# Optimization experiments

Hardware: AMD Instinct MI355X
Metric: run time of the kernel (lower is better)

The kernel has to match this reference:

```python
import jax, jax.numpy as jnp
import numpy as np

B, T, C = 4, 2048, 768
N_HEADS = 16
HEAD_DIM = C // N_HEADS  # 48
ROPE_BASE = 10000.0


def setup_inputs() -> dict:
    key = jax.random.key(0)
    ks = jax.random.split(key, 6)
    s = 0.02
    return {
        "hidden_states": jax.random.normal(ks[0], (B, T, C), dtype=jnp.float32),
        "attention_mask": jnp.ones((B, T), dtype=jnp.float32),
        "Wq": jax.random.normal(ks[1], (C, C), dtype=jnp.float32) * s,
        "bq": jnp.zeros((C,), dtype=jnp.float32),
        "Wk": jax.random.normal(ks[2], (C, C), dtype=jnp.float32) * s,
        "bk": jnp.zeros((C,), dtype=jnp.float32),
        "Wv": jax.random.normal(ks[3], (C, C), dtype=jnp.float32) * s,
        "bv": jnp.zeros((C,), dtype=jnp.float32),
        "Wo": jax.random.normal(ks[4], (C, C), dtype=jnp.float32) * s,
        "bo": jnp.zeros((C,), dtype=jnp.float32),
    }


def _rotate_half(x):
    x1, x2 = jnp.split(x, 2, axis=-1)
    return jnp.concatenate([-x2, x1], axis=-1)


def reference(hidden_states, attention_mask, Wq, bq, Wk, bk, Wv, bv, Wo, bo):
    b, t, c = hidden_states.shape
    h, d = N_HEADS, c // N_HEADS

    def split_heads(x):  # [b,t,c] -> [b,h,t,d]
        return x.reshape(b, t, h, d).transpose(0, 2, 1, 3)

    q = split_heads(hidden_states @ Wq.T + bq)
    k = split_heads(hidden_states @ Wk.T + bk)
    v = split_heads(hidden_states @ Wv.T + bv)

    # rotary embedding: cos/sin [t, d]
    pos = jnp.arange(t, dtype=jnp.float32)
    inv_freq = 1.0 / (ROPE_BASE ** (jnp.arange(0, d, 2, dtype=jnp.float32) / d))
    freqs = pos[:, None] * inv_freq[None, :]          # [t, d/2]
    emb = jnp.concatenate([freqs, freqs], axis=-1)    # [t, d]
    cos, sin = jnp.cos(emb), jnp.sin(emb)
    q = q * cos + _rotate_half(q) * sin
    k = k * cos + _rotate_half(k) * sin

    scores = jnp.einsum('bhqd,bhkd->bhqk', q, k) / jnp.sqrt(jnp.asarray(d, q.dtype))
    # additive padding mask: (1 - mask) * -10000, broadcast [b,1,1,t]
    scores = scores + (1.0 - attention_mask)[:, None, None, :] * -10000.0
    # causal mask with -inf
    causal = jnp.tril(jnp.ones((t, t), dtype=bool))
    scores = jnp.where(causal[None, None], scores, -jnp.inf)

    probs = jax.nn.softmax(scores, axis=-1)
    ctx = jnp.einsum('bhqk,bhkd->bhqd', probs, v)
    ctx = ctx.transpose(0, 2, 1, 3).reshape(b, t, c)
    return ctx @ Wo.T + bo
```

## Files before the change

### kernel.cpp

```cpp
#include <hip/hip_runtime.h>
#include <hip/hip_bf16.h>
#include <math.h>

#define BB 4
#define TT 2048
#define CC 768
#define NHD 16
#define HD 48
#define NQT 32

typedef __hip_bfloat16 bf16;
typedef __attribute__((ext_vector_type(8))) short short8;
typedef __attribute__((ext_vector_type(4))) float floatx4;

__device__ __forceinline__ unsigned short f2bf(float x) {
    bf16 h = __float2bfloat16(x);
    return *(unsigned short*)&h;
}
__device__ __forceinline__ float bfu2f(unsigned short u) {
    return __uint_as_float(((unsigned)u) << 16);
}

__device__ __forceinline__ void gl_lds16(const void* g, void* s) {
    __builtin_amdgcn_global_load_lds((const __attribute__((address_space(1))) void*)g,
                                     (__attribute__((address_space(3))) void*)s, 16, 0, 0);
}

__device__ __forceinline__ unsigned int pk_bf2(float a, float b) {
    unsigned int ua = __float_as_uint(a) + 0x8000u;
    unsigned int ub = __float_as_uint(b) + 0x8000u;
    return __builtin_amdgcn_perm(ub, ua, 0x07060302);
}

__device__ __forceinline__ unsigned int cvtpk(float lo, float hi) {
    unsigned int r;
    asm("v_cvt_pk_bf16_f32 %0, %1, %2" : "=v"(r) : "v"(lo), "v"(hi));
    return r;
}

#define HOT_BARRIER() asm volatile("s_waitcnt lgkmcnt(0)\n\ts_barrier" ::: "memory")

__global__ __launch_bounds__(256) void cast_hs(const float* __restrict__ src,
                                               unsigned short* __restrict__ dst) {
    int i = (blockIdx.x * 256 + threadIdx.x) * 4;
    float4 v = *(const float4*)(src + i);
    ushort4 p;
    p.x = f2bf(v.x); p.y = f2bf(v.y); p.z = f2bf(v.z); p.w = f2bf(v.w);
    *(ushort4*)(dst + i) = p;
}

__global__ __launch_bounds__(256) void cast_w4(const float* __restrict__ s0, const float* __restrict__ s1,
                                               const float* __restrict__ s2, const float* __restrict__ s3,
                                               unsigned short* __restrict__ d0, unsigned short* __restrict__ d1,
                                               unsigned short* __restrict__ d2, unsigned short* __restrict__ d3) {
    const float* s; unsigned short* d;
    switch (blockIdx.y) {
        case 0: s = s0; d = d0; break;
        case 1: s = s1; d = d1; break;
        case 2: s = s2; d = d2; break;
        default: s = s3; d = d3; break;
    }
    int i = (blockIdx.x * 256 + threadIdx.x) * 4;
    float4 v = *(const float4*)(s + i);
    ushort4 p;
    p.x = f2bf(v.x); p.y = f2bf(v.y); p.z = f2bf(v.z); p.w = f2bf(v.w);
    *(ushort4*)(d + i) = p;
}

__global__ __launch_bounds__(256) void rope_table(float2* __restrict__ tab) {
    int idx = blockIdx.x * 256 + threadIdx.x;
    int t = idx / 24, p = idx % 24;
    float inv_freq = powf(10000.0f, -((float)(2 * p) / (float)HD));
    float ang = (float)t * inv_freq;
    float sn, cs;
    sincosf(ang, &sn, &cs);
    tab[idx] = make_float2(cs, sn);
}

template <int MODE>
__global__ __launch_bounds__(256) void gemm_mfma(const unsigned short* __restrict__ A,
                                                 const unsigned short* __restrict__ Bw,
                                                 const float* __restrict__ b0p,
                                                 const float* __restrict__ b1p,
                                                 const float* __restrict__ b2p,
                                                 void* __restrict__ out0,
                                                 void* __restrict__ out1,
                                                 void* __restrict__ out2) {
    __shared__ __align__(16) unsigned short As[128][64];
    __shared__ __align__(16) unsigned short Bs[128][64];
    const int tid = threadIdx.x;
    const int w = tid >> 6, lane = tid & 63;
    const int quad = lane >> 4, ln = lane & 15;
    const int wr = w >> 1, wc = w & 1;

    const int NXB = (MODE == 1) ? 18 : 6;
    const int bx = blockIdx.x;
    const int xcd = bx & 7, slot = bx >> 3;
    const int n0 = (slot % NXB) * 128;
    const int m0 = ((slot / NXB) * 8 + xcd) * 128;

    const int srow = lane >> 3;
    const int ssw = ((lane & 7) ^ srow) * 8;
    const unsigned short* agp[4];
    const unsigned short* bgp[4];
    void* asl[4];
    void* bsl[4];
#pragma unroll
    for (int i = 0; i < 4; ++i) {
        const int R = i * 32 + w * 8;
        agp[i] = A + (size_t)(m0 + R + srow) * CC + ssw;
        bgp[i] = Bw + (size_t)(n0 + R + srow) * CC + ssw;
        asl[i] = &As[R][0];
        bsl[i] = &Bs[R][0];
    }

    floatx4 acc[4][4];
#pragma unroll
    for (int mi = 0; mi < 4; ++mi)
#pragma unroll
        for (int ni = 0; ni < 4; ++ni) acc[mi][ni] = (floatx4){0.f, 0.f, 0.f, 0.f};

    const int ps0 = (quad ^ (ln & 7)) * 8;

    for (int k0 = 0; k0 < CC; k0 += 64) {
        __syncthreads();
#pragma unroll
        for (int i = 0; i < 4; ++i) {
            gl_lds16(agp[i] + k0, asl[i]);
            gl_lds16(bgp[i] + k0, bsl[i]);
        }
        __syncthreads();
#pragma unroll
        for (int kh = 0; kh < 2; ++kh) {
            const int ps = ps0 ^ (kh * 32);
            short8 af[4], bfr[4];
#pragma unroll
            for (int mi = 0; mi < 4; ++mi)
                af[mi] = *(const short8*)&As[wr * 64 + mi * 16 + ln][ps];
#pragma unroll
            for (int ni = 0; ni < 4; ++ni)
                bfr[ni] = *(const short8*)&Bs[wc * 64 + ni * 16 + ln][ps];
#pragma unroll
            for (int mi = 0; mi < 4; ++mi)
#pragma unroll
                for (int ni = 0; ni < 4; ++ni)
                    acc[mi][ni] = __builtin_amdgcn_mfma_f32_16x16x32_bf16(af[mi], bfr[ni], acc[mi][ni], 0, 0, 0);
        }
    }

    if (MODE == 0) {
        float* outf = (float*)out0;
        float bv[4];
#pragma unroll
        for (int ni = 0; ni < 4; ++ni) bv[ni] = b0p[n0 + wc * 64 + ni * 16 + ln];
#pragma unroll
        for (int mi = 0; mi < 4; ++mi)
#pragma unroll
            for (int r = 0; r < 4; ++r) {
                size_t row = m0 + wr * 64 + mi * 16 + quad * 4 + r;
#pragma unroll
                for (int ni = 0; ni < 4; ++ni)
                    outf[row * CC + n0 + wc * 64 + ni * 16 + ln] = acc[mi][ni][r] + bv[ni];
            }
    } else {
        const int seg = n0 / CC;
        const int nl0 = n0 - seg * CC;
        const float* bp = (seg == 0) ? b0p : (seg == 1) ? b1p : b2p;
        float bv[4];
#pragma unroll
        for (int ni = 0; ni < 4; ++ni) bv[ni] = bp[nl0 + wc * 64 + ni * 16 + ln];

        if (seg < 2) {
            unsigned short* outb = (unsigned short*)(seg == 0 ? out0 : out1);
#pragma unroll
            for (int mi = 0; mi < 4; ++mi)
#pragma unroll
                for (int r = 0; r < 4; ++r) {
                    size_t row = m0 + wr * 64 + mi * 16 + quad * 4 + r;
#pragma unroll
                    for (int ni = 0; ni < 4; ++ni)
                        outb[row * CC + nl0 + wc * 64 + ni * 16 + ln] = f2bf(acc[mi][ni][r] + bv[ni]);
                }
        } else {
            unsigned short* outb = (unsigned short*)out2;
            const int b = m0 >> 11;
#pragma unroll
            for (int ni = 0; ni < 4; ++ni) {
                int col = nl0 + wc * 64 + ni * 16 + ln;
                int h = col / HD, d = col % HD;
                size_t base = (size_t)((b * NHD + h) * HD + d) * TT;
#pragma unroll
                for (int mi = 0; mi < 4; ++mi) {
                    int t = (m0 & 2047) + wr * 64 + mi * 16 + quad * 4;
                    ushort4 pk;
                    pk.x = f2bf(acc[mi][ni][0] + bv[ni]);
                    pk.y = f2bf(acc[mi][ni][1] + bv[ni]);
                    pk.z = f2bf(acc[mi][ni][2] + bv[ni]);
                    pk.w = f2bf(acc[mi][ni][3] + bv[ni]);
                    *(ushort4*)(outb + base + t) = pk;
                }
            }
        }
    }
}

__global__ __launch_bounds__(256) void rope_bf(unsigned short* __restrict__ q,
                                               unsigned short* __restrict__ k,
                                               const float2* __restrict__ tab) {
    int idx = blockIdx.x * blockDim.x + threadIdx.x;
    const int HALF = HD / 2;
    int p8 = idx % 3;
    int rest = idx / 3;
    int h = rest % NHD;
    int n = rest / NHD;
    int t = n & (TT - 1);
    const float QSC = 0.14433756729740643f * 1.4426950408889634f;
    size_t base = (size_t)n * CC + h * HD + p8 * 8;
    const float2* tp = tab + t * HALF + p8 * 8;

    short8 q1 = *(const short8*)(q + base);
    short8 q2 = *(const short8*)(q + base + HALF);
    short8 k1 = *(const short8*)(k + base);
    short8 k2 = *(const short8*)(k + base + HALF);
    short8 r1, r2, s1, s2;
#pragma unroll
    for (int jj = 0; jj < 8; ++jj) {
        float2 cssn = tp[jj];
        float cs = cssn.x, sn = cssn.y;
        float a = bfu2f((unsigned short)q1[jj]), bb = bfu2f((unsigned short)q2[jj]);
        r1[jj] = (short)f2bf((a * cs - bb * sn) * QSC);
        r2[jj] = (short)f2bf((bb * cs + a * sn) * QSC);
        float c2 = bfu2f((unsigned short)k1[jj]), d2 = bfu2f((unsigned short)k2[jj]);
        s1[jj] = (short)f2bf(c2 * cs - d2 * sn);
        s2[jj] = (short)f2bf(d2 * cs + c2 * sn);
    }
    *(short8*)(q + base) = r1;
    *(short8*)(q + base + HALF) = r2;
    *(short8*)(k + base) = s1;
    *(short8*)(k + base + HALF) = s2;
}

__global__ __launch_bounds__(128, 2) void attn_kernel(const unsigned short* __restrict__ qb,
                                                      const unsigned short* __restrict__ kb,
                                                      const unsigned short* __restrict__ vt,
                                                      const float* __restrict__ amask,
                                                      unsigned short* __restrict__ ctx) {
    const int bx = blockIdx.x;
    const int xcd = bx & 7;
    const int s = bx >> 3;
    const int bh_l = s & 7;
    const int pairidx = s >> 3;
    const int j = (bh_l << 3) | xcd;
    const int b = j >> 4, h = j & 15;
    const int tid = threadIdx.x;
    const int w = tid >> 6, lane = tid & 63;
    const int g = lane >> 4, ln = lane & 15;
    const int sw = ln & 7;

    __shared__ __align__(16) unsigned short Ks[2][64][64];
    __shared__ __align__(16) unsigned short Vs[2][48][64];
    __shared__ __align__(16) unsigned short Pw[2][32][64];
    __shared__ __align__(16) float l_s[2][32];

    const short8 z8 = {0, 0, 0, 0, 0, 0, 0, 0};
    const short8 ones8 = {0x3F80, 0x3F80, 0x3F80, 0x3F80, 0x3F80, 0x3F80, 0x3F80, 0x3F80};

    {
        int rr = tid & 63, half = tid >> 6;
        *(short8*)&Ks[0][rr][((6 + half) ^ (rr & 7)) * 8] = z8;
        *(short8*)&Ks[1][rr][((6 + half) ^ (rr & 7)) * 8] = z8;
    }

    const int u0 = tid, u1 = tid + 128, u2 = tid + 256;
    const int rK0 = u0 / 6, sK0 = u0 % 6;
    const int rK1 = u1 / 6, sK1 = u1 % 6;
    const int rK2 = u2 / 6, sK2 = u2 % 6;
    const int rV0 = u0 >> 3, sV0 = u0 & 7;
    const int rV1 = u1 >> 3, sV1 = u1 & 7;
    const int rV2 = u2 >> 3, sV2 = u2 & 7;
    const int offK0 = rK0 * 64 + (sK0 ^ (rK0 & 7)) * 8;
    const int offK1 = rK1 * 64 + (sK1 ^ (rK1 & 7)) * 8;
    const int offK2 = rK2 * 64 + (sK2 ^ (rK2 & 7)) * 8;
    const int offV0 = rV0 * 64 + (sV0 ^ (rV0 & 7)) * 8;
    const int offV1 = rV1 * 64 + (sV1 ^ (rV1 & 7)) * 8;
    const int offV2 = rV2 * 64 + (sV2 ^ (rV2 & 7)) * 8;
    const int offM = (tid & 63) * 64 + (6 ^ (tid & 7)) * 8;

    const unsigned short* kbase0 = kb + (size_t)(b * TT + rK0) * CC + h * HD + sK0 * 8;
    const unsigned short* kbase1 = kb + (size_t)(b * TT + rK1) * CC + h * HD + sK1 * 8;
    const unsigned short* kbase2 = kb + (size_t)(b * TT + rK2) * CC + h * HD + sK2 * 8;
    const unsigned short* vbase0 = vt + ((size_t)((b * NHD + h) * HD) + rV0) * TT + sV0 * 8;
    const unsigned short* vbase1 = vt + ((size_t)((b * NHD + h) * HD) + rV1) * TT + sV1 * 8;
    const unsigned short* vbase2 = vt + ((size_t)((b * NHD + h) * HD) + rV2) * TT + sV2 * 8;
    const float* mbase = amask + b * TT + (tid & 63);
    const float MBS = -10000.0f * 1.4426950408889634f;
    const short8 vone = (ln == 0) ? ones8 : z8;
    const int rowA = w * 32 + ln;

    for (int rep = 0; rep < 2; ++rep) {
        const int qt = rep ? (NQT - 1 - pairidx) : pairidx;
        const int q0 = qt * 64;

        const unsigned short* qrA = qb + (size_t)(b * TT + q0 + w * 32 + ln) * CC + h * HD;
        const unsigned short* qrB = qrA + (size_t)16 * CC;
        short8 aq0a = *(const short8*)(qrA + g * 8);
        short8 aq0b = *(const short8*)(qrB + g * 8);
        short8 aq1a, aq1b;
        if (g < 2) {
            aq1a = *(const short8*)(qrA + 32 + g * 8);
            aq1b = *(const short8*)(qrB + 32 + g * 8);
        } else {
            aq1a = z8; aq1b = z8;
            if (g == 2) { aq1a[0] = (short)0x3F80; aq1b[0] = (short)0x3F80; }
        }

        const unsigned short* kp0 = kbase0;
        const unsigned short* kp1 = kbase1;
        const unsigned short* kp2 = kbase2;
        const unsigned short* vp0 = vbase0;
        const unsigned short* vp1 = vbase1;
        const unsigned short* vp2 = vbase2;
        const float* mp = mbase;

        short8 kr0 = *(const short8*)kp0;
        short8 kr1 = *(const short8*)kp1;
        short8 kr2 = *(const short8*)kp2;
        short8 vr0 = *(const short8*)vp0;
        short8 vr1 = *(const short8*)vp1;
        short8 vr2 = *(const short8*)vp2;
        float mr = (tid < 64) ? *mp : 1.0f;

        HOT_BARRIER();
        {
            unsigned short* kd = &Ks[0][0][0];
            unsigned short* vd = &Vs[0][0][0];
            *(short8*)(kd + offK0) = kr0;
            *(short8*)(kd + offK1) = kr1;
            *(short8*)(kd + offK2) = kr2;
            *(short8*)(vd + offV0) = vr0;
            *(short8*)(vd + offV1) = vr1;
            *(short8*)(vd + offV2) = vr2;
            if (tid < 64) kd[offM] = f2bf((1.0f - mr) * MBS);
        }
        HOT_BARRIER();

        floatx4 oa0 = {0.f, 0.f, 0.f, 0.f}, oa1 = oa0, oa2 = oa0, oa3 = oa0;
        floatx4 ob0 = oa0, ob1 = oa0, ob2 = oa0, ob3 = oa0;

        for (int kt = 0; kt <= qt; ++kt) {
            const int buf = kt & 1;

            if (kt < qt) {
                kp0 += (size_t)64 * CC; kr0 = *(const short8*)kp0;
                kp1 += (size_t)64 * CC; kr1 = *(const short8*)kp1;
                kp2 += (size_t)64 * CC; kr2 = *(const short8*)kp2;
                vp0 += 64; vr0 = *(const short8*)vp0;
                vp1 += 64; vr1 = *(const short8*)vp1;
                vp2 += 64; vr2 = *(const short8*)vp2;
                if (tid < 64) { mp += 64; mr = *mp; }
            }

            const bool masked = (kt == qt);

            floatx4 sa_[4], sb_[4];
#pragma unroll
            for (int c = 0; c < 4; ++c) {
                short8 kf0 = *(const short8*)&Ks[buf][c * 16 + ln][(g ^ sw) * 8];
                short8 kf1 = *(const short8*)&Ks[buf][c * 16 + ln][((4 + g) ^ sw) * 8];
                floatx4 z = {0.f, 0.f, 0.f, 0.f};
                floatx4 za = __builtin_amdgcn_mfma_f32_16x16x32_bf16(kf0, aq0a, z, 0, 0, 0);
                sa_[c] = __builtin_amdgcn_mfma_f32_16x16x32_bf16(kf1, aq1a, za, 0, 0, 0);
                floatx4 zb = __builtin_amdgcn_mfma_f32_16x16x32_bf16(kf0, aq0b, z, 0, 0, 0);
                sb_[c] = __builtin_amdgcn_mfma_f32_16x16x32_bf16(kf1, aq1b, zb, 0, 0, 0);
            }

#pragma unroll
            for (int c = 0; c < 4; ++c) {
                float pva[4], pvb[4];
#pragma unroll
                for (int r = 0; r < 4; ++r) {
                    pva[r] = __builtin_amdgcn_exp2f(sa_[c][r]);
                    pvb[r] = __builtin_amdgcn_exp2f(sb_[c][r]);
                }
                if (masked) {
#pragma unroll
                    for (int r = 0; r < 4; ++r) {
                        int kcol = c * 16 + g * 4 + r;
                        if (kcol > rowA) pva[r] = 0.f;
                        if (kcol > rowA + 16) pvb[r] = 0.f;
                    }
                }
                uint2 pka, pkb;
                pka.x = cvtpk(pva[0], pva[1]);
                pka.y = cvtpk(pva[2], pva[3]);
                pkb.x = cvtpk(pvb[0], pvb[1]);
                pkb.y = cvtpk(pvb[2], pvb[3]);
                *(uint2*)&Pw[w][ln][((2 * c + (g >> 1)) ^ sw) * 8 + (g & 1) * 4] = pka;
                *(uint2*)&Pw[w][16 + ln][((2 * c + (g >> 1)) ^ sw) * 8 + (g & 1) * 4] = pkb;
            }

            short8 pa0a = *(const short8*)&Pw[w][ln][(g ^ sw) * 8];
            short8 pa1a = *(const short8*)&Pw[w][ln][((4 + g) ^ sw) * 8];
            short8 pa0b = *(const short8*)&Pw[w][16 + ln][(g ^ sw) * 8];
            short8 pa1b = *(const short8*)&Pw[w][16 + ln][((4 + g) ^ sw) * 8];

#pragma unroll
            for (int n = 0; n < 3; ++n) {
                short8 vb0 = *(const short8*)&Vs[buf][n * 16 + ln][(g ^ sw) * 8];
                short8 vb1 = *(const short8*)&Vs[buf][n * 16 + ln][((4 + g) ^ sw) * 8];
                floatx4 acc = (n == 0) ? oa0 : (n == 1) ? oa1 : oa2;
                acc = __builtin_amdgcn_mfma_f32_16x16x32_bf16(pa0a, vb0, acc, 0, 0, 0);
                acc = __builtin_amdgcn_mfma_f32_16x16x32_bf16(pa1a, vb1, acc, 0, 0, 0);
                if (n == 0) oa0 = acc; else if (n == 1) oa1 = acc; else oa2 = acc;
                floatx4 accb = (n == 0) ? ob0 : (n == 1) ? ob1 : ob2;
                accb = __builtin_amdgcn_mfma_f32_16x16x32_bf16(pa0b, vb0, accb, 0, 0, 0);
                accb = __builtin_amdgcn_mfma_f32_16x16x32_bf16(pa1b, vb1, accb, 0, 0, 0);
                if (n == 0) ob0 = accb; else if (n == 1) ob1 = accb; else ob2 = accb;
            }
            oa3 = __builtin_amdgcn_mfma_f32_16x16x32_bf16(pa0a, vone, oa3, 0, 0, 0);
            oa3 = __builtin_amdgcn_mfma_f32_16x16x32_bf16(pa1a, vone, oa3, 0, 0, 0);
            ob3 = __builtin_amdgcn_mfma_f32_16x16x32_bf16(pa0b, vone, ob3, 0, 0, 0);
            ob3 = __builtin_amdgcn_mfma_f32_16x16x32_bf16(pa1b, vone, ob3, 0, 0, 0);

            if (kt < qt) {
                unsigned short* kd = &Ks[buf ^ 1][0][0];
                unsigned short* vd = &Vs[buf ^ 1][0][0];
                *(short8*)(kd + offK0) = kr0;
                *(short8*)(kd + offK1) = kr1;
                *(short8*)(kd + offK2) = kr2;
                *(short8*)(vd + offV0) = vr0;
                *(short8*)(vd + offV1) = vr1;
                *(short8*)(vd + offV2) = vr2;
                if (tid < 64) kd[offM] = f2bf((1.0f - mr) * MBS);
            }
            HOT_BARRIER();
        }

        if (ln == 0) {
            *(floatx4*)&l_s[w][g * 4] = oa3;
            *(floatx4*)&l_s[w][16 + g * 4] = ob3;
        }
        floatx4 l4a = *(const floatx4*)&l_s[w][g * 4];
        floatx4 l4b = *(const floatx4*)&l_s[w][16 + g * 4];
#pragma unroll
        for (int r = 0; r < 4; ++r) {
            float invA = 1.0f / l4a[r];
            int t = q0 + w * 32 + g * 4 + r;
            unsigned short* dst = ctx + (size_t)(b * TT + t) * CC + h * HD;
            dst[ln] = f2bf(oa0[r] * invA);
            dst[16 + ln] = f2bf(oa1[r] * invA);
            dst[32 + ln] = f2bf(oa2[r] * invA);
            float invB = 1.0f / l4b[r];
            unsigned short* dstB = dst + (size_t)16 * CC;
            dstB[ln] = f2bf(ob0[r] * invB);
            dstB[16 + ln] = f2bf(ob1[r] * invB);
            dstB[32 + ln] = f2bf(ob2[r] * invB);
        }
    }
}

extern "C" void kernel_launch(void* const* d_in, const int* in_sizes, int n_in,
                              void* d_out, int out_size, void* d_ws, size_t ws_size,
                              hipStream_t stream) {
    const float* hs = (const float*)d_in[0];
    const float* amask = (const float*)d_in[1];
    const float* Wq = (const float*)d_in[2];
    const float* bq = (const float*)d_in[3];
    const float* Wk = (const float*)d_in[4];
    const float* bk = (const float*)d_in[5];
    const float* Wv = (const float*)d_in[6];
    const float* bv = (const float*)d_in[7];
    const float* Wo = (const float*)d_in[8];
    const float* bo = (const float*)d_in[9];

    const size_t NELEM = (size_t)BB * TT * CC;
    const size_t WELEM = (size_t)CC * CC;
    unsigned short* hb  = (unsigned short*)d_ws;
    unsigned short* qbuf = hb + NELEM;
    unsigned short* kbuf = qbuf + NELEM;
    unsigned short* vtb = kbuf + NELEM;
    unsigned short* ctxb = vtb + NELEM;
    unsigned short* wqb = ctxb + NELEM;
    unsigned short* wkb = wqb + WELEM;
    unsigned short* wvb = wkb + WELEM;
    unsigned short* wob = wvb + WELEM;
    float2* ropetab = (float2*)(wob + WELEM);

    cast_hs<<<NELEM / 1024, 256, 0, stream>>>(hs, hb);
    dim3 wgrid(WELEM / 1024, 4);
    cast_w4<<<wgrid, 256, 0, stream>>>(Wq, Wk, Wv, Wo, wqb, wkb, wvb, wob);
    rope_table<<<(TT * (HD / 2)) / 256, 256, 0, stream>>>(ropetab);

    gemm_mfma<1><<<18 * 64, 256, 0, stream>>>(hb, wqb, bq, bk, bv, qbuf, kbuf, vtb);

    int rope_total = BB * TT * NHD * 3;
    rope_bf<<<rope_total / 256, 256, 0, stream>>>(qbuf, kbuf, ropetab);

    attn_kernel<<<1024, 128, 0, stream>>>(qbuf, kbuf, vtb, amask, ctxb);

    gemm_mfma<0><<<6 * 64, 256, 0, stream>>>(ctxb, wob, bo, nullptr, nullptr,
                                             (float*)d_out, nullptr, nullptr);
}
```

Baseline: 223.9 us.

## Switch attention to 32x32x16 MFMA and build P fragments in registers

```diff
diff --git a/kernel.cpp b/kernel.cpp
--- a/kernel.cpp
+++ b/kernel.cpp
@@ -12,6 +12,8 @@
 typedef __hip_bfloat16 bf16;
 typedef __attribute__((ext_vector_type(8))) short short8;
 typedef __attribute__((ext_vector_type(4))) float floatx4;
+typedef __attribute__((ext_vector_type(16))) float floatx16;
+typedef __attribute__((ext_vector_type(2))) unsigned int uintx2;
 
 __device__ __forceinline__ unsigned short f2bf(float x) {
     bf16 h = __float2bfloat16(x);
@@ -24,18 +26,25 @@
 __device__ __forceinline__ void gl_lds16(const void* g, void* s) {
     __builtin_amdgcn_global_load_lds((const __attribute__((address_space(1))) void*)g,
                                      (__attribute__((address_space(3))) void*)s, 16, 0, 0);
-}
-
-__device__ __forceinline__ unsigned int pk_bf2(float a, float b) {
-    unsigned int ua = __float_as_uint(a) + 0x8000u;
-    unsigned int ub = __float_as_uint(b) + 0x8000u;
-    return __builtin_amdgcn_perm(ub, ua, 0x07060302);
 }
 
 __device__ __forceinline__ unsigned int cvtpk(float lo, float hi) {
     unsigned int r;
     asm("v_cvt_pk_bf16_f32 %0, %1, %2" : "=v"(r) : "v"(lo), "v"(hi));
     return r;
+}
+
+__device__ __forceinline__ short8 build_pfrag(float p0, float p1, float p2, float p3,
+                                              float p4, float p5, float p6, float p7) {
+    unsigned int a = cvtpk(p0, p1);
+    unsigned int b = cvtpk(p4, p5);
+    unsigned int c = cvtpk(p2, p3);
+    unsigned int d = cvtpk(p6, p7);
+    uintx2 s1 = __builtin_amdgcn_permlane32_swap(a, b, false, false);
+    uintx2 s2 = __builtin_amdgcn_permlane32_swap(c, d, false, false);
+    union { unsigned int u[4]; short8 s; } r;
+    r.u[0] = s1[0]; r.u[1] = s2[0]; r.u[2] = s1[1]; r.u[3] = s2[1];
+    return r.s;
 }
 
 #define HOT_BARRIER() asm volatile("s_waitcnt lgkmcnt(0)\n\ts_barrier" ::: "memory")
@@ -254,13 +263,11 @@
     const int b = j >> 4, h = j & 15;
     const int tid = threadIdx.x;
     const int w = tid >> 6, lane = tid & 63;
-    const int g = lane >> 4, ln = lane & 15;
-    const int sw = ln & 7;
+    const int l5 = lane & 31, hi = lane >> 5;
 
     __shared__ __align__(16) unsigned short Ks[2][64][64];
-    __shared__ __align__(16) unsigned short Vs[2][48][64];
-    __shared__ __align__(16) unsigned short Pw[2][32][64];
-    __shared__ __align__(16) float l_s[2][32];
+    __shared__ __align__(16) unsigned short Vs[2][64][64];
+    __shared__ __align__(16) float l_s[2][2][16];
 
     const short8 z8 = {0, 0, 0, 0, 0, 0, 0, 0};
     const short8 ones8 = {0x3F80, 0x3F80, 0x3F80, 0x3F80, 0x3F80, 0x3F80, 0x3F80, 0x3F80};
@@ -269,6 +276,10 @@
         int rr = tid & 63, half = tid >> 6;
         *(short8*)&Ks[0][rr][((6 + half) ^ (rr & 7)) * 8] = z8;
         *(short8*)&Ks[1][rr][((6 + half) ^ (rr & 7)) * 8] = z8;
+        int vr = 48 + (tid >> 3), vu = tid & 7;
+        short8 pv = (vr == 48) ? ones8 : z8;
+        *(short8*)&Vs[0][vr][vu * 8] = pv;
+        *(short8*)&Vs[1][vr][vu * 8] = pv;
     }
 
     const int u0 = tid, u1 = tid + 128, u2 = tid + 256;
@@ -294,25 +305,19 @@
     const unsigned short* vbase2 = vt + ((size_t)((b * NHD + h) * HD) + rV2) * TT + sV2 * 8;
     const float* mbase = amask + b * TT + (tid & 63);
     const float MBS = -10000.0f * 1.4426950408889634f;
-    const short8 vone = (ln == 0) ? ones8 : z8;
-    const int rowA = w * 32 + ln;
+    const int swz = l5 & 7;
 
     for (int rep = 0; rep < 2; ++rep) {
         const int qt = rep ? (NQT - 1 - pairidx) : pairidx;
         const int q0 = qt * 64;
 
-        const unsigned short* qrA = qb + (size_t)(b * TT + q0 + w * 32 + ln) * CC + h * HD;
-        const unsigned short* qrB = qrA + (size_t)16 * CC;
-        short8 aq0a = *(const short8*)(qrA + g * 8);
-        short8 aq0b = *(const short8*)(qrB + g * 8);
-        short8 aq1a, aq1b;
-        if (g < 2) {
-            aq1a = *(const short8*)(qrA + 32 + g * 8);
-            aq1b = *(const short8*)(qrB + 32 + g * 8);
-        } else {
-            aq1a = z8; aq1b = z8;
-            if (g == 2) { aq1a[0] = (short)0x3F80; aq1b[0] = (short)0x3F80; }
-        }
+        const unsigned short* qr = qb + (size_t)(b * TT + q0 + w * 32 + l5) * CC + h * HD + hi * 8;
+        short8 qf[4];
+        qf[0] = *(const short8*)(qr);
+        qf[1] = *(const short8*)(qr + 16);
+        qf[2] = *(const short8*)(qr + 32);
+        qf[3] = z8;
+        if (hi == 0) qf[3][0] = (short)0x3F80;
 
         const unsigned short* kp0 = kbase0;
         const unsigned short* kp1 = kbase1;
@@ -344,11 +349,14 @@
         }
         HOT_BARRIER();
 
-        floatx4 oa0 = {0.f, 0.f, 0.f, 0.f}, oa1 = oa0, oa2 = oa0, oa3 = oa0;
-        floatx4 ob0 = oa0, ob1 = oa0, ob2 = oa0, ob3 = oa0;
+        floatx16 oA = (floatx16){0.f, 0.f, 0.f, 0.f, 0.f, 0.f, 0.f, 0.f,
+                                 0.f, 0.f, 0.f, 0.f, 0.f, 0.f, 0.f, 0.f};
+        floatx16 oB = oA;
 
         for (int kt = 0; kt <= qt; ++kt) {
             const int buf = kt & 1;
+            const unsigned short* ksb = &Ks[buf][0][0];
+            const unsigned short* vsb = &Vs[buf][0][0];
 
             if (kt < qt) {
                 kp0 += (size_t)64 * CC; kr0 = *(const short8*)kp0;
@@ -360,67 +368,53 @@
                 if (tid < 64) { mp += 64; mr = *mp; }
             }
 
-            const bool masked = (kt == qt);
-
-            floatx4 sa_[4], sb_[4];
-#pragma unroll
-            for (int c = 0; c < 4; ++c) {
-                short8 kf0 = *(const short8*)&Ks[buf][c * 16 + ln][(g ^ sw) * 8];
-                short8 kf1 = *(const short8*)&Ks[buf][c * 16 + ln][((4 + g) ^ sw) * 8];
-                floatx4 z = {0.f, 0.f, 0.f, 0.f};
-                floatx4 za = __builtin_amdgcn_mfma_f32_16x16x32_bf16(kf0, aq0a, z, 0, 0, 0);
-                sa_[c] = __builtin_amdgcn_mfma_f32_16x16x32_bf16(kf1, aq1a, za, 0, 0, 0);
-                floatx4 zb = __builtin_amdgcn_mfma_f32_16x16x32_bf16(kf0, aq0b, z, 0, 0, 0);
-                sb_[c] = __builtin_amdgcn_mfma_f32_16x16x32_bf16(kf1, aq1b, zb, 0, 0, 0);
-            }
-
-#pragma unroll
-            for (int c = 0; c < 4; ++c) {
-                float pva[4], pvb[4];
-#pragma unroll
-                for (int r = 0; r < 4; ++r) {
-                    pva[r] = __builtin_amdgcn_exp2f(sa_[c][r]);
-                    pvb[r] = __builtin_amdgcn_exp2f(sb_[c][r]);
+            floatx16 sc0 = (floatx16){0.f, 0.f, 0.f, 0.f, 0.f, 0.f, 0.f, 0.f,
+                                      0.f, 0.f, 0.f, 0.f, 0.f, 0.f, 0.f, 0.f};
+            floatx16 sc1 = sc0;
+#pragma unroll
+            for (int i = 0; i < 4; ++i) {
+                short8 kf0 = *(const short8*)(ksb + (size_t)l5 * 64 + ((2 * i + hi) ^ swz) * 8);
+                short8 kf1 = *(const short8*)(ksb + (size_t)(32 + l5) * 64 + ((2 * i + hi) ^ swz) * 8);
+                sc0 = __builtin_amdgcn_mfma_f32_32x32x16_bf16(kf0, qf[i], sc0, 0, 0, 0);
+                sc1 = __builtin_amdgcn_mfma_f32_32x32x16_bf16(kf1, qf[i], sc1, 0, 0, 0);
+            }
+
+            short8 vA[4], vB[4];
+#pragma unroll
+            for (int kb2 = 0; kb2 < 4; ++kb2) {
+                vA[kb2] = *(const short8*)(vsb + (size_t)l5 * 64 + ((kb2 * 2 + hi) ^ swz) * 8);
+                vB[kb2] = *(const short8*)(vsb + (size_t)(32 + l5) * 64 + ((kb2 * 2 + hi) ^ swz) * 8);
+            }
+
+            float p0[16], p1[16];
+#pragma unroll
+            for (int r = 0; r < 16; ++r) {
+                p0[r] = __builtin_amdgcn_exp2f(sc0[r]);
+                p1[r] = __builtin_amdgcn_exp2f(sc1[r]);
+            }
+            if (kt == qt) {
+                const int qrl = w * 32 + l5;
+#pragma unroll
+                for (int r = 0; r < 16; ++r) {
+                    int cr = (r & 3) + 8 * (r >> 2) + 4 * hi;
+                    if (cr > qrl) p0[r] = 0.f;
+                    if (32 + cr > qrl) p1[r] = 0.f;
                 }
-                if (masked) {
-#pragma unroll
-                    for (int r = 0; r < 4; ++r) {
-                        int kcol = c * 16 + g * 4 + r;
-                        if (kcol > rowA) pva[r] = 0.f;
-                        if (kcol > rowA + 16) pvb[r] = 0.f;
-                    }
-                }
-                uint2 pka, pkb;
-                pka.x = cvtpk(pva[0], pva[1]);
-                pka.y = cvtpk(pva[2], pva[3]);
-                pkb.x = cvtpk(pvb[0], pvb[1]);
-                pkb.y = cvtpk(pvb[2], pvb[3]);
-                *(uint2*)&Pw[w][ln][((2 * c + (g >> 1)) ^ sw) * 8 + (g & 1) * 4] = pka;
-                *(uint2*)&Pw[w][16 + ln][((2 * c + (g >> 1)) ^ sw) * 8 + (g & 1) * 4] = pkb;
-            }
-
-            short8 pa0a = *(const short8*)&Pw[w][ln][(g ^ sw) * 8];
-            short8 pa1a = *(const short8*)&Pw[w][ln][((4 + g) ^ sw) * 8];
-            short8 pa0b = *(const short8*)&Pw[w][16 + ln][(g ^ sw) * 8];
-            short8 pa1b = *(const short8*)&Pw[w][16 + ln][((4 + g) ^ sw) * 8];
-
-#pragma unroll
-            for (int n = 0; n < 3; ++n) {
-                short8 vb0 = *(const short8*)&Vs[buf][n * 16 + ln][(g ^ sw) * 8];
-                short8 vb1 = *(const short8*)&Vs[buf][n * 16 + ln][((4 + g) ^ sw) * 8];
-                floatx4 acc = (n == 0) ? oa0 : (n == 1) ? oa1 : oa2;
-                acc = __builtin_amdgcn_mfma_f32_16x16x32_bf16(pa0a, vb0, acc, 0, 0, 0);
-                acc = __builtin_amdgcn_mfma_f32_16x16x32_bf16(pa1a, vb1, acc, 0, 0, 0);
-                if (n == 0) oa0 = acc; else if (n == 1) oa1 = acc; else oa2 = acc;
-                floatx4 accb = (n == 0) ? ob0 : (n == 1) ? ob1 : ob2;
-                accb = __builtin_amdgcn_mfma_f32_16x16x32_bf16(pa0b, vb0, accb, 0, 0, 0);
-                accb = __builtin_amdgcn_mfma_f32_16x16x32_bf16(pa1b, vb1, accb, 0, 0, 0);
-                if (n == 0) ob0 = accb; else if (n == 1) ob1 = accb; else ob2 = accb;
-            }
-            oa3 = __builtin_amdgcn_mfma_f32_16x16x32_bf16(pa0a, vone, oa3, 0, 0, 0);
-            oa3 = __builtin_amdgcn_mfma_f32_16x16x32_bf16(pa1a, vone, oa3, 0, 0, 0);
-            ob3 = __builtin_amdgcn_mfma_f32_16x16x32_bf16(pa0b, vone, ob3, 0, 0, 0);
-            ob3 = __builtin_amdgcn_mfma_f32_16x16x32_bf16(pa1b, vone, ob3, 0, 0, 0);
+            }
+
+            short8 pa0 = build_pfrag(p0[0], p0[1], p0[2], p0[3], p0[4], p0[5], p0[6], p0[7]);
+            short8 pa1 = build_pfrag(p0[8], p0[9], p0[10], p0[11], p0[12], p0[13], p0[14], p0[15]);
+            short8 pa2 = build_pfrag(p1[0], p1[1], p1[2], p1[3], p1[4], p1[5], p1[6], p1[7]);
+            short8 pa3 = build_pfrag(p1[8], p1[9], p1[10], p1[11], p1[12], p1[13], p1[14], p1[15]);
+
+            oA = __builtin_amdgcn_mfma_f32_32x32x16_bf16(pa0, vA[0], oA, 0, 0, 0);
+            oB = __builtin_amdgcn_mfma_f32_32x32x16_bf16(pa0, vB[0], oB, 0, 0, 0);
+            oA = __builtin_amdgcn_mfma_f32_32x32x16_bf16(pa1, vA[1], oA, 0, 0, 0);
+            oB = __builtin_amdgcn_mfma_f32_32x32x16_bf16(pa1, vB[1], oB, 0, 0, 0);
+            oA = __builtin_amdgcn_mfma_f32_32x32x16_bf16(pa2, vA[2], oA, 0, 0, 0);
+            oB = __builtin_amdgcn_mfma_f32_32x32x16_bf16(pa2, vB[2], oB, 0, 0, 0);
+            oA = __builtin_amdgcn_mfma_f32_32x32x16_bf16(pa3, vA[3], oA, 0, 0, 0);
+            oB = __builtin_amdgcn_mfma_f32_32x32x16_bf16(pa3, vB[3], oB, 0, 0, 0);
 
             if (kt < qt) {
                 unsigned short* kd = &Ks[buf ^ 1][0][0];
@@ -436,25 +430,19 @@
             HOT_BARRIER();
         }
 
-        if (ln == 0) {
-            *(floatx4*)&l_s[w][g * 4] = oa3;
-            *(floatx4*)&l_s[w][16 + g * 4] = ob3;
-        }
-        floatx4 l4a = *(const floatx4*)&l_s[w][g * 4];
-        floatx4 l4b = *(const floatx4*)&l_s[w][16 + g * 4];
-#pragma unroll
-        for (int r = 0; r < 4; ++r) {
-            float invA = 1.0f / l4a[r];
-            int t = q0 + w * 32 + g * 4 + r;
+        if (l5 == 16) {
+#pragma unroll
+            for (int r = 0; r < 16; ++r) l_s[w][hi][r] = oB[r];
+        }
+        asm volatile("s_waitcnt lgkmcnt(0)" ::: "memory");
+
+#pragma unroll
+        for (int r = 0; r < 16; ++r) {
+            float inv_l = 1.0f / l_s[w][hi][r];
+            int t = q0 + w * 32 + ((r & 3) + 8 * (r >> 2) + 4 * hi);
             unsigned short* dst = ctx + (size_t)(b * TT + t) * CC + h * HD;
-            dst[ln] = f2bf(oa0[r] * invA);
-            dst[16 + ln] = f2bf(oa1[r] * invA);
-            dst[32 + ln] = f2bf(oa2[r] * invA);
-            float invB = 1.0f / l4b[r];
-            unsigned short* dstB = dst + (size_t)16 * CC;
-            dstB[ln] = f2bf(ob0[r] * invB);
-            dstB[16 + ln] = f2bf(ob1[r] * invB);
-            dstB[32 + ln] = f2bf(ob2[r] * invB);
+            dst[l5] = f2bf(oA[r] * inv_l);
+            if (l5 < 16) dst[32 + l5] = f2bf(oB[r] * inv_l);
         }
     }
 }
```

Result: no change. 223.6 us (-0.1%).
